# Performance work log

Measured on AMD Instinct MI355X. Metric: run time of the kernel, lower is better.

Reference implementation:

```python
import jax, jax.numpy as jnp
import numpy as np

S, B, D, NH, DH, L, V, DI = 1024, 4, 768, 12, 64, 4, 32000, 3072


def layer_norm(x, g, b, eps=1e-5):
    mu = jnp.mean(x, axis=-1, keepdims=True)
    var = jnp.mean((x - mu) ** 2, axis=-1, keepdims=True)
    return (x - mu) * jax.lax.rsqrt(var + eps) * g + b


def sinusoid_pos_emb():
    # PositionalEmbedding: ger(pos_seq, inv_freq) then [sin, cos]
    pos_seq = jnp.arange(S - 1, -1, -1, dtype=jnp.float32)
    inv_freq = 1.0 / (10000.0 ** (jnp.arange(0.0, D, 2.0) / D))
    si = pos_seq[:, None] * inv_freq[None, :]
    return jnp.concatenate([jnp.sin(si), jnp.cos(si)], axis=-1)  # (S, D)


def setup_inputs() -> dict:
    key = jax.random.key(0)
    ks = jax.random.split(key, 16)
    w = 0.02
    inp = jax.random.randint(ks[0], (S, B), 0, V)
    word_emb = jax.random.normal(ks[1], (V, D)) * w
    Wq = jax.random.normal(ks[2], (L, D, D)) * w
    Wkv = jax.random.normal(ks[3], (L, 2 * D, D)) * w
    Wo = jax.random.normal(ks[4], (L, D, D)) * w
    ln1_g = jnp.ones((L, D)); ln1_b = jnp.zeros((L, D))
    ffW1 = jax.random.normal(ks[5], (L, DI, D)) * w
    ffb1 = jnp.zeros((L, DI))
    ffW2 = jax.random.normal(ks[6], (L, D, DI)) * w
    ffb2 = jnp.zeros((L, D))
    ln2_g = jnp.ones((L, D)); ln2_b = jnp.zeros((L, D))
    # pre-populated InfiniAttn memory state; norm kept strictly positive
    memory = jax.random.normal(ks[7], (L, B, NH, DH, DH)) * jnp.sqrt(jnp.float32(S))
    mem_norm = jax.random.uniform(ks[8], (L, B, NH, DH)) * S + 0.5 * S
    return dict(inp=inp, word_emb=word_emb, Wq=Wq, Wkv=Wkv, Wo=Wo,
                ln1_g=ln1_g, ln1_b=ln1_b, ffW1=ffW1, ffb1=ffb1,
                ffW2=ffW2, ffb2=ffb2, ln2_g=ln2_g, ln2_b=ln2_b,
                memory=memory, mem_norm=mem_norm)


def reference(inp, word_emb, Wq, Wkv, Wo, ln1_g, ln1_b, ffW1, ffb1, ffW2, ffb2,
              ln2_g, ln2_b, memory, mem_norm):
    emb_scale = D ** 0.5
    h = word_emb[inp] * emb_scale + sinusoid_pos_emb()[:, None, :]  # (S,B,D)
    causal = jnp.triu(jnp.ones((S, S), dtype=bool), k=1)  # mask j > i
    scale = 1.0 / DH ** 0.5
    gate = jax.nn.sigmoid(jnp.float32(0.01))  # sigmoid(beta), beta_eps=0.01 (buffer)
    neg_inf = jnp.finfo(h.dtype).min
    new_mems, new_norms = [], []
    for l in range(L):
        q = (h @ Wq[l].T).reshape(S, B, NH, DH)
        kv = h @ Wkv[l].T
        k, v = jnp.split(kv, 2, axis=-1)
        k = k.reshape(S, B, NH, DH)
        v = v.reshape(S, B, NH, DH)
        score = jnp.einsum('ibnd,jbnd->ijbn', q, k) * scale
        score = jnp.where(causal[:, :, None, None], neg_inf, score)
        prob = jax.nn.softmax(score, axis=1)
        attn_vec = jnp.einsum('ijbn,jbnd->ibnd', prob, v).reshape(S, B, NH * DH)
        # NOTE: original calls _update_memory(head_q, head_v, head_k), i.e. K=v, V=k
        Qb = jnp.swapaxes(q, 0, 1)  # (B,S,n,d)
        Kb = jnp.swapaxes(v, 0, 1)
        Vb = jnp.swapaxes(k, 0, 1)
        cQ = jax.nn.elu(Qb) + 1.0
        cK = jax.nn.elu(Kb) + 1.0
        # memory retrieval (detached in the original)
        num = jnp.einsum('bsnk,bnkv->bsnv', cQ, memory[l])
        den = jnp.einsum('bsnk,bnk->bsn', cQ, mem_norm[l])[..., None]
        content_A = jax.lax.stop_gradient(num / den)  # (B,S,n,d)
        # memory update with delta trick (no_grad in the original)
        numK = jnp.einsum('bsnk,bnkv->bsnv', cK, memory[l])
        denK = jnp.einsum('bsnk,bnk->bsn', cK, mem_norm[l])[..., None]
        delta = numK / denK
        new_mems.append(jax.lax.stop_gradient(
            memory[l] + jnp.einsum('bsnk,bsnv->bnkv', cK, Vb - delta)))
        new_norms.append(jax.lax.stop_gradient(mem_norm[l] + cK.sum(axis=1)))
        # gated injection of memory content into local attention output
        attn_vec = gate * jnp.swapaxes(content_A, 0, 1).reshape(S, B, NH * DH) \
                   + (1.0 - gate) * attn_vec
        out = layer_norm(h + attn_vec @ Wo[l].T, ln1_g[l], ln1_b[l])
        core = jax.nn.relu(out @ ffW1[l].T + ffb1[l]) @ ffW2[l].T + ffb2[l]
        h = layer_norm(out + core, ln2_g[l], ln2_b[l])
    return h, jnp.stack(new_mems), jnp.stack(new_norms)
```

## Files before the change

kernel.cpp:

```cpp
#include <hip/hip_runtime.h>
#include <hip/hip_bf16.h>
#include <math.h>

#define S 1024
#define B 4
#define Dm 768
#define NH 12
#define DH 64
#define NL 4
#define DI 3072
#define QS 2304
#define MU_CHUNK 8

typedef __hip_bfloat16 bf16;
typedef short bf16x8 __attribute__((ext_vector_type(8)));
typedef float f32x4 __attribute__((ext_vector_type(4)));

__device__ __forceinline__ float b2f(bf16 x) { return __bfloat162float(x); }
__device__ __forceinline__ bf16 f2b(float x) { return __float2bfloat16(x); }

__device__ __forceinline__ float ldv(const float* p, size_t i) { return p[i]; }
__device__ __forceinline__ float ldv(const bf16* p, size_t i) { return b2f(p[i]); }

__device__ __forceinline__ float wave_sum(float x) {
  #pragma unroll
  for (int off = 32; off > 0; off >>= 1) x += __shfl_xor(x, off, 64);
  return x;
}

typedef const __attribute__((address_space(1))) unsigned int guint;
typedef __attribute__((address_space(3))) unsigned int luint;
__device__ __forceinline__ void async_cp16(const void* g, void* l) {
  __builtin_amdgcn_global_load_lds((guint*)g, (luint*)l, 16, 0, 0);
}

__global__ void embed_kernel(const int* __restrict__ inp, const float* __restrict__ wemb,
                             float* __restrict__ h, bf16* __restrict__ hb) {
  int idx = blockIdx.x * blockDim.x + threadIdx.x;
  if (idx >= S * B * Dm) return;
  int d = idx % Dm;
  int sb = idx / Dm;
  int b = sb % B;
  int s = sb / B;
  int tok = inp[s * B + b];
  float e = wemb[(size_t)tok * Dm + d] * 27.712812921102035f;
  float ps = (float)(S - 1 - s);
  float pe;
  if (d < Dm / 2) {
    float invf = expf(-(2.0f * (float)d / (float)Dm) * 9.210340371976184f);
    pe = sinf(ps * invf);
  } else {
    int j = d - Dm / 2;
    float invf = expf(-(2.0f * (float)j / (float)Dm) * 9.210340371976184f);
    pe = cosf(ps * invf);
  }
  float val = e + pe;
  h[idx] = val;
  hb[idx] = f2b(val);
}

#define SEG_QKV 1769472
#define SEG_WO  2359296
#define SEG_W1  4718592
#define SEG_END 7077888
__global__ void convw_kernel(const float* __restrict__ Wq, const float* __restrict__ Wkv,
                             const float* __restrict__ Wo, const float* __restrict__ W1,
                             const float* __restrict__ W2, bf16* __restrict__ dst) {
  int idx = (blockIdx.x * blockDim.x + threadIdx.x) * 4;
  if (idx >= SEG_END) return;
  const float* src;
  if (idx < SEG_QKV) {
    src = (idx < 589824) ? Wq + idx : Wkv + (idx - 589824);
  } else if (idx < SEG_WO) {
    src = Wo + (idx - SEG_QKV);
  } else if (idx < SEG_W1) {
    src = W1 + (idx - SEG_WO);
  } else {
    src = W2 + (idx - SEG_W1);
  }
  float4 f = *(const float4*)src;
  bf16 b0 = f2b(f.x), b1 = f2b(f.y), b2 = f2b(f.z), b3 = f2b(f.w);
  unsigned short o[4];
  o[0] = *(unsigned short*)&b0; o[1] = *(unsigned short*)&b1;
  o[2] = *(unsigned short*)&b2; o[3] = *(unsigned short*)&b3;
  *(uint2*)((unsigned short*)dst + idx) = *(uint2*)o;
}

template <int MREP, int RELU>
__global__ __launch_bounds__(256) void gemm_async(const bf16* __restrict__ A,
                                                  const bf16* __restrict__ W,
                                                  const float* __restrict__ bias,
                                                  bf16* __restrict__ C,
                                                  int ldc, int K) {
  constexpr int BM = MREP * 32;
  __shared__ __align__(16) unsigned short Asm[BM * 32];
  __shared__ __align__(16) unsigned short Bsm[128 * 32];
  const int t = threadIdx.x;
  const int w = t >> 6, lane = t & 63;
  const int col = lane & 15, quad = lane >> 4;
  const int wm = w >> 1, wn = w & 1;
  const int m0 = blockIdx.y * BM, n0 = blockIdx.x * 128;

  const bf16* aSrc = A + (size_t)(m0 + w * 16 + col) * K + quad * 8;
  const bf16* bSrc = W + (size_t)(n0 + w * 16 + col) * K + quad * 8;

  const f32x4 zf = {0.0f, 0.0f, 0.0f, 0.0f};
  f32x4 acc[MREP][4];
  #pragma unroll
  for (int mt = 0; mt < MREP; mt++)
    #pragma unroll
    for (int nt = 0; nt < 4; nt++) acc[mt][nt] = zf;

  for (int kk = 0; kk < K; kk += 32) {
    __syncthreads();
    #pragma unroll
    for (int i = 0; i < MREP / 2; i++)
      async_cp16(aSrc + kk + (size_t)i * 64 * K, &Asm[i * 2048 + w * 512]);
    #pragma unroll
    for (int i = 0; i < 2; i++)
      async_cp16(bSrc + kk + (size_t)i * 64 * K, &Bsm[i * 2048 + w * 512]);
    __syncthreads();
    bf16x8 af[MREP], bfr[4];
    #pragma unroll
    for (int mt = 0; mt < MREP; mt++)
      af[mt] = *(const bf16x8*)&Asm[(wm * MREP + mt) * 512 + lane * 8];
    #pragma unroll
    for (int nt = 0; nt < 4; nt++)
      bfr[nt] = *(const bf16x8*)&Bsm[(wn * 4 + nt) * 512 + lane * 8];
    #pragma unroll
    for (int mt = 0; mt < MREP; mt++)
      #pragma unroll
      for (int nt = 0; nt < 4; nt++)
        acc[mt][nt] = __builtin_amdgcn_mfma_f32_16x16x32_bf16(af[mt], bfr[nt],
                                                              acc[mt][nt], 0, 0, 0);
  }

  #pragma unroll
  for (int nt = 0; nt < 4; nt++) {
    const int colg = n0 + wn * 64 + nt * 16 + col;
    const float bv = bias ? bias[colg] : 0.0f;
    #pragma unroll
    for (int mt = 0; mt < MREP; mt++) {
      #pragma unroll
      for (int r = 0; r < 4; r++) {
        const int row = m0 + wm * (MREP * 16) + mt * 16 + quad * 4 + r;
        float val = acc[mt][nt][r] + bv;
        if (RELU) val = fmaxf(val, 0.0f);
        C[(size_t)row * ldc + colg] = f2b(val);
      }
    }
  }
}

__global__ __launch_bounds__(256) void attn_flash(const bf16* __restrict__ q,
                                                  const bf16* __restrict__ k,
                                                  const bf16* __restrict__ v,
                                                  bf16* __restrict__ att) {
  const int it = blockIdx.x;
  const int bn = blockIdx.y;
  const int b = bn / NH, n = bn % NH;
  const int t = threadIdx.x;
  const int w = t >> 6, lane = t & 63;
  const int col = lane & 15, quad = lane >> 4;
  const int i0 = it * 64;

  __shared__ __align__(16) unsigned short Kt[64 * 72];
  __shared__ __align__(16) unsigned short Vt[64 * 72];
  __shared__ __align__(16) unsigned short Pw[64 * 72];

  const unsigned short* qp = (const unsigned short*)q;
  const unsigned short* kp = (const unsigned short*)k;
  const unsigned short* vp = (const unsigned short*)v;

  bf16x8 aq[2];
  {
    size_t qb = ((size_t)(i0 + w * 16 + col) * B + b) * QS + n * DH + quad * 8;
    aq[0] = *(const bf16x8*)(qp + qb);
    aq[1] = *(const bf16x8*)(qp + qb + 32);
  }

  const f32x4 zf = {0.0f, 0.0f, 0.0f, 0.0f};
  float mrow[4], lrow[4];
  f32x4 o[4];
  #pragma unroll
  for (int r = 0; r < 4; r++) { mrow[r] = -1e30f; lrow[r] = 0.0f; }
  #pragma unroll
  for (int db = 0; db < 4; db++) o[db] = zf;

  const int jj = t >> 2;
  const int d0 = (t & 3) << 4;

  for (int jt = 0; jt <= it; jt++) {
    const int j0 = jt * 64;
    __syncthreads();
    {
      size_t gb = ((size_t)(j0 + jj) * B + b) * QS + n * DH + d0;
      *(uint4*)&Kt[jj * 72 + d0] = *(const uint4*)(kp + gb);
      *(uint4*)&Kt[jj * 72 + d0 + 8] = *(const uint4*)(kp + gb + 8);
      unsigned short tv[16];
      *(uint4*)tv = *(const uint4*)(vp + gb);
      *(uint4*)(tv + 8) = *(const uint4*)(vp + gb + 8);
      #pragma unroll
      for (int x = 0; x < 16; x++) Vt[(d0 + x) * 72 + jj] = tv[x];
    }
    __syncthreads();

    f32x4 sf[4];
    #pragma unroll
    for (int nb = 0; nb < 4; nb++) sf[nb] = zf;
    #pragma unroll
    for (int ks = 0; ks < 2; ks++) {
      #pragma unroll
      for (int nb = 0; nb < 4; nb++) {
        bf16x8 kb = *(const bf16x8*)&Kt[(nb * 16 + col) * 72 + ks * 32 + quad * 8];
        sf[nb] = __builtin_amdgcn_mfma_f32_16x16x32_bf16(aq[ks], kb, sf[nb], 0, 0, 0);
      }
    }

    const bool diag = (jt == it);
    #pragma unroll
    for (int r = 0; r < 4; r++) {
      const int irow = i0 + w * 16 + quad * 4 + r;
      float sv[4];
      #pragma unroll
      for (int nb = 0; nb < 4; nb++) {
        float s = sf[nb][r] * 0.125f;
        if (diag && (j0 + nb * 16 + col) > irow) s = -1e30f;
        sv[nb] = s;
      }
      float rm = fmaxf(fmaxf(sv[0], sv[1]), fmaxf(sv[2], sv[3]));
      #pragma unroll
      for (int off = 8; off > 0; off >>= 1) rm = fmaxf(rm, __shfl_xor(rm, off, 64));
      const float mn = fmaxf(mrow[r], rm);
      const float alpha = __expf(mrow[r] - mn);
      mrow[r] = mn;
      float ps = 0.0f;
      #pragma unroll
      for (int nb = 0; nb < 4; nb++) {
        float p = __expf(sv[nb] - mn);
        ps += p;
        bf16 hb = f2b(p);
        Pw[(w * 16 + quad * 4 + r) * 72 + nb * 16 + col] = *(unsigned short*)&hb;
      }
      #pragma unroll
      for (int off = 8; off > 0; off >>= 1) ps += __shfl_xor(ps, off, 64);
      lrow[r] = lrow[r] * alpha + ps;
      #pragma unroll
      for (int db = 0; db < 4; db++) o[db][r] *= alpha;
    }

    #pragma unroll
    for (int ks = 0; ks < 2; ks++) {
      bf16x8 pa = *(const bf16x8*)&Pw[(w * 16 + col) * 72 + ks * 32 + quad * 8];
      #pragma unroll
      for (int db = 0; db < 4; db++) {
        bf16x8 vb = *(const bf16x8*)&Vt[(db * 16 + col) * 72 + ks * 32 + quad * 8];
        o[db] = __builtin_amdgcn_mfma_f32_16x16x32_bf16(pa, vb, o[db], 0, 0, 0);
      }
    }
  }

  unsigned short* ap = (unsigned short*)att;
  #pragma unroll
  for (int r = 0; r < 4; r++) {
    const int irow = i0 + w * 16 + quad * 4 + r;
    const float inv = 1.0f / lrow[r];
    size_t ob = ((size_t)irow * B + b) * Dm + n * DH + col;
    #pragma unroll
    for (int db = 0; db < 4; db++) {
      bf16 hb = f2b(o[db][r] * inv);
      ap[ob + db * 16] = *(unsigned short*)&hb;
    }
  }
}

__global__ __launch_bounds__(256) void meminfer_mfma(const bf16* __restrict__ qkv,
                                                     const float* __restrict__ mem,
                                                     const float* __restrict__ mnorm,
                                                     bf16* __restrict__ att,
                                                     bf16* __restrict__ vd) {
  const int s0 = blockIdx.x * 64;
  const int bn = blockIdx.y;
  const int b = bn / NH, n = bn % NH;
  const int t = threadIdx.x;
  const int w = t >> 6, lane = t & 63;
  const int col = lane & 15, quad = lane >> 4;

  __shared__ __align__(16) unsigned short CQ[4096];
  __shared__ __align__(16) unsigned short CK[4096];
  __shared__ __align__(16) unsigned short Bm[5120];

  const unsigned short* qp = (const unsigned short*)qkv;

  {
    int r = t >> 2;
    int k0 = (t & 3) * 16;
    size_t gb = ((size_t)(s0 + r) * B + b) * QS + n * DH + k0;
    int abase = (r >> 4) * 1024 + (k0 >> 5) * 512 + ((k0 & 31) >> 3) * 128 + (r & 15) * 8;
    unsigned short tq[16], tv[16], oq[16], ov[16];
    *(uint4*)tq = *(const uint4*)(qp + gb);
    *(uint4*)(tq + 8) = *(const uint4*)(qp + gb + 8);
    *(uint4*)tv = *(const uint4*)(qp + gb + 1536);
    *(uint4*)(tv + 8) = *(const uint4*)(qp + gb + 1536 + 8);
    #pragma unroll
    for (int i = 0; i < 16; i++) {
      float fq = b2f(*(const bf16*)&tq[i]);
      float fv = b2f(*(const bf16*)&tv[i]);
      float eq = fq > 0.0f ? fq + 1.0f : __expf(fq);
      float ev = fv > 0.0f ? fv + 1.0f : __expf(fv);
      bf16 bq = f2b(eq), bv2 = f2b(ev);
      oq[i] = *(unsigned short*)&bq;
      ov[i] = *(unsigned short*)&bv2;
    }
    *(bf16x8*)&CQ[abase] = *(bf16x8*)oq;
    *(bf16x8*)&CQ[abase + 128] = *(bf16x8*)(oq + 8);
    *(bf16x8*)&CK[abase] = *(bf16x8*)ov;
    *(bf16x8*)&CK[abase + 128] = *(bf16x8*)(ov + 8);
  }
  {
    int v = t & 63, kb = (t >> 6) * 16;
    const float* mp = mem + (size_t)bn * DH * DH;
    #pragma unroll
    for (int i = 0; i < 16; i++) {
      int k = kb + i;
      bf16 mb = f2b(mp[(size_t)k * DH + v]);
      int addr = (v >> 4) * 1024 + (k >> 5) * 512 + ((k & 31) >> 3) * 128 + (v & 15) * 8 + (k & 7);
      Bm[addr] = *(unsigned short*)&mb;
    }
  }
  {
    int a = t * 4;
    int m = (a >> 3) & 15;
    int kk = (a >> 9) * 32 + ((a >> 7) & 3) * 8 + (a & 7);
    unsigned short vals[4] = {0, 0, 0, 0};
    if (m == 0) {
      const float* np = mnorm + (size_t)bn * DH;
      #pragma unroll
      for (int j = 0; j < 4; j++) {
        bf16 nb = f2b(np[kk + j]);
        vals[j] = *(unsigned short*)&nb;
      }
    }
    *(uint2*)&Bm[4096 + a] = *(uint2*)vals;
  }
  __syncthreads();

  const f32x4 zf = {0.0f, 0.0f, 0.0f, 0.0f};
  f32x4 aq[5], ak[5];
  #pragma unroll
  for (int nb = 0; nb < 5; nb++) { aq[nb] = zf; ak[nb] = zf; }
  #pragma unroll
  for (int ks = 0; ks < 2; ks++) {
    bf16x8 fq = *(const bf16x8*)&CQ[w * 1024 + ks * 512 + lane * 8];
    bf16x8 fk = *(const bf16x8*)&CK[w * 1024 + ks * 512 + lane * 8];
    #pragma unroll
    for (int nb = 0; nb < 5; nb++) {
      bf16x8 bm = *(const bf16x8*)&Bm[nb * 1024 + ks * 512 + lane * 8];
      aq[nb] = __builtin_amdgcn_mfma_f32_16x16x32_bf16(fq, bm, aq[nb], 0, 0, 0);
      ak[nb] = __builtin_amdgcn_mfma_f32_16x16x32_bf16(fk, bm, ak[nb], 0, 0, 0);
    }
  }

  const float gate = 1.0f / (1.0f + expf(-0.01f));
  unsigned short* ap = (unsigned short*)att;
  unsigned short* vp2 = (unsigned short*)vd;
  #pragma unroll
  for (int r = 0; r < 4; r++) {
    const int srow = s0 + w * 16 + quad * 4 + r;
    const float denq = __shfl(aq[4][r], lane & 48, 64);
    const float denk = __shfl(ak[4][r], lane & 48, 64);
    const size_t bd = ((size_t)srow * B + b) * Dm + n * DH + col;
    const size_t bq = ((size_t)srow * B + b) * QS + 768 + n * DH + col;
    #pragma unroll
    for (int nb = 0; nb < 4; nb++) {
      float content = aq[nb][r] / denq;
      float delta = ak[nb][r] / denk;
      float attv = b2f(*(const bf16*)&ap[bd + nb * 16]);
      bf16 ao = f2b(gate * content + (1.0f - gate) * attv);
      ap[bd + nb * 16] = *(unsigned short*)&ao;
      float kvv = b2f(*(const bf16*)&qp[bq + nb * 16]);
      bf16 vo = f2b(kvv - delta);
      vp2[bd + nb * 16] = *(unsigned short*)&vo;
    }
  }
}

__global__ void memupd_kernel(const bf16* __restrict__ qkv, const bf16* __restrict__ vd,
                              float* __restrict__ part, float* __restrict__ pnorm) {
  int bn = blockIdx.x % (B * NH);
  int c = blockIdx.x / (B * NH);
  int b = bn / NH, n = bn % NH;
  int t = threadIdx.x;
  int k = t >> 2;
  int v0 = (t & 3) * 16;
  __shared__ float ckl[8][DH];
  __shared__ float vdl[8][DH];
  float acc[16];
  #pragma unroll
  for (int j = 0; j < 16; j++) acc[j] = 0.0f;
  float nsum = 0.0f;
  const int sBeg = c * (S / MU_CHUNK), sEnd = sBeg + S / MU_CHUNK;
  for (int s0 = sBeg; s0 < sEnd; s0 += 8) {
    #pragma unroll
    for (int i2 = 0; i2 < 2; i2++) {
      int idx = t + i2 * 256;
      int sp = idx >> 6, dd = idx & 63;
      int gq = ((s0 + sp) * B + b) * QS + 1536 + n * DH + dd;
      int gd = ((s0 + sp) * B + b) * Dm + n * DH + dd;
      float vv = b2f(qkv[gq]);
      ckl[sp][dd] = vv > 0.0f ? vv + 1.0f : expf(vv);
      vdl[sp][dd] = b2f(vd[gd]);
    }
    __syncthreads();
    #pragma unroll
    for (int sp = 0; sp < 8; sp++) {
      float cc = ckl[sp][k];
      if ((t & 3) == 0) nsum += cc;
      #pragma unroll
      for (int j = 0; j < 16; j++) acc[j] += cc * vdl[sp][v0 + j];
    }
    __syncthreads();
  }
  float* prow = part + (size_t)c * (B * NH * DH * DH) + (size_t)bn * DH * DH;
  #pragma unroll
  for (int j4 = 0; j4 < 4; j4++) {
    float4 o;
    o.x = acc[j4 * 4 + 0]; o.y = acc[j4 * 4 + 1];
    o.z = acc[j4 * 4 + 2]; o.w = acc[j4 * 4 + 3];
    *(float4*)&prow[k * DH + v0 + j4 * 4] = o;
  }
  if ((t & 3) == 0) pnorm[(size_t)c * (B * NH * DH) + bn * DH + k] = nsum;
}

__global__ void memred_kernel(const float* __restrict__ mem, const float* __restrict__ mnorm,
                              const float* __restrict__ part, const float* __restrict__ pnorm,
                              float* __restrict__ out_mem, float* __restrict__ out_norm) {
  const int MEMN = B * NH * DH * DH;
  int i = blockIdx.x * blockDim.x + threadIdx.x;
  if (i < MEMN / 4) {
    int i4 = i * 4;
    float4 a = *(const float4*)(mem + i4);
    #pragma unroll
    for (int c = 0; c < MU_CHUNK; c++) {
      float4 p = *(const float4*)(part + (size_t)c * MEMN + i4);
      a.x += p.x; a.y += p.y; a.z += p.z; a.w += p.w;
    }
    *(float4*)(out_mem + i4) = a;
  } else {
    int j4 = (i - MEMN / 4) * 4;
    if (j4 < B * NH * DH) {
      float4 a = *(const float4*)(mnorm + j4);
      #pragma unroll
      for (int c = 0; c < MU_CHUNK; c++) {
        float4 p = *(const float4*)(pnorm + (size_t)c * (B * NH * DH) + j4);
        a.x += p.x; a.y += p.y; a.z += p.z; a.w += p.w;
      }
      *(float4*)(out_norm + j4) = a;
    }
  }
}

template <typename TX, typename TY>
__global__ void addln_kernel(const TX* __restrict__ x, const TY* __restrict__ y,
                             const float* __restrict__ g, const float* __restrict__ bb,
                             float* __restrict__ outf, bf16* __restrict__ outb) {
  int row = blockIdx.x;
  int t = threadIdx.x;
  float vals[3];
  float sum = 0.0f, sq = 0.0f;
  #pragma unroll
  for (int i = 0; i < 3; i++) {
    size_t idx = (size_t)row * Dm + t + i * 256;
    float vv = ldv(x, idx) + ldv(y, idx);
    vals[i] = vv;
    sum += vv;
    sq += vv * vv;
  }
  sum = wave_sum(sum);
  sq = wave_sum(sq);
  __shared__ float s1[4], s2[4];
  int w = t >> 6, lane = t & 63;
  if (lane == 0) { s1[w] = sum; s2[w] = sq; }
  __syncthreads();
  if (t == 0) {
    s1[0] = s1[0] + s1[1] + s1[2] + s1[3];
    s2[0] = s2[0] + s2[1] + s2[2] + s2[3];
  }
  __syncthreads();
  sum = s1[0]; sq = s2[0];
  float mu = sum / 768.0f;
  float var = sq / 768.0f - mu * mu;
  float rs = rsqrtf(var + 1e-5f);
  #pragma unroll
  for (int i = 0; i < 3; i++) {
    int d = t + i * 256;
    float o = (vals[i] - mu) * rs * g[d] + bb[d];
    size_t idx = (size_t)row * Dm + d;
    if (outf) outf[idx] = o;
    if (outb) outb[idx] = f2b(o);
  }
}

extern "C" void kernel_launch(void* const* d_in, const int* in_sizes, int n_in,
                              void* d_out, int out_size, void* d_ws, size_t ws_size,
                              hipStream_t stream) {
  (void)in_sizes; (void)n_in; (void)out_size; (void)ws_size;
  const int*   inp   = (const int*)d_in[0];
  const float* wemb  = (const float*)d_in[1];
  const float* Wq    = (const float*)d_in[2];
  const float* Wkv   = (const float*)d_in[3];
  const float* Wo    = (const float*)d_in[4];
  const float* ln1g  = (const float*)d_in[5];
  const float* ln1b  = (const float*)d_in[6];
  const float* fW1   = (const float*)d_in[7];
  const float* fb1   = (const float*)d_in[8];
  const float* fW2   = (const float*)d_in[9];
  const float* fb2   = (const float*)d_in[10];
  const float* ln2g  = (const float*)d_in[11];
  const float* ln2b  = (const float*)d_in[12];
  const float* mem   = (const float*)d_in[13];
  const float* mnorm = (const float*)d_in[14];

  const size_t SBD = (size_t)S * B * Dm;

  bf16* ws   = (bf16*)d_ws;
  bf16* qkv  = ws;
  bf16* vd   = ws + 3 * SBD;
  bf16* att  = ws + 4 * SBD;
  bf16* hbf  = att;
  bf16* ff2o = att;
  bf16* out1 = ws + 5 * SBD;
  bf16* wb   = ws + 6 * SBD;
  bf16* ffm  = ws;
  bf16* tmp  = ws;
  float* part  = (float*)out1;
  float* pnorm = (float*)(wb + SEG_END);

  float* h    = (float*)d_out;
  float* outm = h + SBD;
  float* outn = outm + (size_t)NL * B * NH * DH * DH;

  dim3 b256(256);
  embed_kernel<<<dim3((S * B * Dm + 255) / 256), b256, 0, stream>>>(inp, wemb, h, hbf);

  for (int l = 0; l < NL; l++) {
    convw_kernel<<<dim3(SEG_END / 4 / 256), b256, 0, stream>>>(
        Wq + (size_t)l * Dm * Dm, Wkv + (size_t)l * 2 * Dm * Dm,
        Wo + (size_t)l * Dm * Dm, fW1 + (size_t)l * DI * Dm,
        fW2 + (size_t)l * Dm * DI, wb);
    const bf16* wqkv = wb;
    const bf16* wo_b = wb + SEG_QKV;
    const bf16* w1_b = wb + SEG_WO;
    const bf16* w2_b = wb + SEG_W1;
    const float* mem_l = mem + (size_t)l * B * NH * DH * DH;
    const float* mn_l  = mnorm + (size_t)l * B * NH * DH;
    float* outm_l = outm + (size_t)l * B * NH * DH * DH;
    float* outn_l = outn + (size_t)l * B * NH * DH;

    gemm_async<4, 0><<<dim3(QS / 128, 32), b256, 0, stream>>>(hbf, wqkv, nullptr, qkv, QS, Dm);

    attn_flash<<<dim3(S / 64, B * NH), b256, 0, stream>>>(qkv, qkv + 768, qkv + 1536, att);
    meminfer_mfma<<<dim3(S / 64, B * NH), b256, 0, stream>>>(qkv, mem_l, mn_l, att, vd);
    memupd_kernel<<<dim3(B * NH * MU_CHUNK), b256, 0, stream>>>(qkv, vd, part, pnorm);
    memred_kernel<<<dim3(771), b256, 0, stream>>>(mem_l, mn_l, part, pnorm, outm_l, outn_l);

    gemm_async<2, 0><<<dim3(Dm / 128, 64), b256, 0, stream>>>(att, wo_b, nullptr, tmp, Dm, Dm);
    addln_kernel<float, bf16><<<dim3(S * B), b256, 0, stream>>>(
        h, tmp, ln1g + l * Dm, ln1b + l * Dm, nullptr, out1);

    gemm_async<4, 1><<<dim3(DI / 128, 32), b256, 0, stream>>>(out1, w1_b, fb1 + (size_t)l * DI,
                                                              ffm, DI, Dm);
    gemm_async<2, 0><<<dim3(Dm / 128, 64), b256, 0, stream>>>(ffm, w2_b, fb2 + (size_t)l * Dm,
                                                              ff2o, Dm, DI);
    addln_kernel<bf16, bf16><<<dim3(S * B), b256, 0, stream>>>(
        out1, ff2o, ln2g + l * Dm, ln2b + l * Dm, h, hbf);
  }
}
```

Measured before the change: 1.375 ms.

## Double-buffer GEMM shared tiles and add split-K for narrow-output GEMMs

The GEMM kernel now double-buffers its A and B shared-memory tiles, so the async copy for the next K step is issued before the MFMAs on the current tile, with one barrier per iteration instead of two. The Wo and FFN2 GEMMs, which have only 6x64 output tiles, are split over K into two slices that write fp32 partial sums. A separate reduce kernel adds the slices, applies the bias and converts to bf16. This aims to hide load latency and put more blocks on the device, at the cost of extra fp32 partial-sum traffic, an extra launch per split GEMM, and double the LDS per block.

```diff
diff --git a/kernel.cpp b/kernel.cpp
--- a/kernel.cpp
+++ b/kernel.cpp
@@ -86,23 +86,25 @@
   *(uint2*)((unsigned short*)dst + idx) = *(uint2*)o;
 }
 
-template <int MREP, int RELU>
+template <int MREP, int RELU, int SPLITK, typename OT>
 __global__ __launch_bounds__(256) void gemm_async(const bf16* __restrict__ A,
                                                   const bf16* __restrict__ W,
                                                   const float* __restrict__ bias,
-                                                  bf16* __restrict__ C,
+                                                  OT* __restrict__ C,
                                                   int ldc, int K) {
   constexpr int BM = MREP * 32;
-  __shared__ __align__(16) unsigned short Asm[BM * 32];
-  __shared__ __align__(16) unsigned short Bsm[128 * 32];
+  __shared__ __align__(16) unsigned short Asm[2][BM * 32];
+  __shared__ __align__(16) unsigned short Bsm[2][128 * 32];
   const int t = threadIdx.x;
   const int w = t >> 6, lane = t & 63;
   const int col = lane & 15, quad = lane >> 4;
   const int wm = w >> 1, wn = w & 1;
   const int m0 = blockIdx.y * BM, n0 = blockIdx.x * 128;
-
-  const bf16* aSrc = A + (size_t)(m0 + w * 16 + col) * K + quad * 8;
-  const bf16* bSrc = W + (size_t)(n0 + w * 16 + col) * K + quad * 8;
+  const int Kc = K / SPLITK;
+  const int kbeg = (SPLITK > 1) ? blockIdx.z * Kc : 0;
+
+  const bf16* aSrc = A + (size_t)(m0 + w * 16 + col) * K + kbeg + quad * 8;
+  const bf16* bSrc = W + (size_t)(n0 + w * 16 + col) * K + kbeg + quad * 8;
 
   const f32x4 zf = {0.0f, 0.0f, 0.0f, 0.0f};
   f32x4 acc[MREP][4];
@@ -111,30 +113,57 @@
     #pragma unroll
     for (int nt = 0; nt < 4; nt++) acc[mt][nt] = zf;
 
-  for (int kk = 0; kk < K; kk += 32) {
-    __syncthreads();
+  #pragma unroll
+  for (int i = 0; i < MREP / 2; i++)
+    async_cp16(aSrc + (size_t)i * 64 * K, &Asm[0][i * 2048 + w * 512]);
+  #pragma unroll
+  for (int i = 0; i < 2; i++)
+    async_cp16(bSrc + (size_t)i * 64 * K, &Bsm[0][i * 2048 + w * 512]);
+  __syncthreads();
+
+  int cur = 0;
+  for (int kk = 32; kk < Kc; kk += 32) {
     #pragma unroll
     for (int i = 0; i < MREP / 2; i++)
-      async_cp16(aSrc + kk + (size_t)i * 64 * K, &Asm[i * 2048 + w * 512]);
+      async_cp16(aSrc + kk + (size_t)i * 64 * K, &Asm[cur ^ 1][i * 2048 + w * 512]);
     #pragma unroll
     for (int i = 0; i < 2; i++)
-      async_cp16(bSrc + kk + (size_t)i * 64 * K, &Bsm[i * 2048 + w * 512]);
-    __syncthreads();
+      async_cp16(bSrc + kk + (size_t)i * 64 * K, &Bsm[cur ^ 1][i * 2048 + w * 512]);
     bf16x8 af[MREP], bfr[4];
     #pragma unroll
     for (int mt = 0; mt < MREP; mt++)
-      af[mt] = *(const bf16x8*)&Asm[(wm * MREP + mt) * 512 + lane * 8];
+      af[mt] = *(const bf16x8*)&Asm[cur][(wm * MREP + mt) * 512 + lane * 8];
     #pragma unroll
     for (int nt = 0; nt < 4; nt++)
-      bfr[nt] = *(const bf16x8*)&Bsm[(wn * 4 + nt) * 512 + lane * 8];
+      bfr[nt] = *(const bf16x8*)&Bsm[cur][(wn * 4 + nt) * 512 + lane * 8];
     #pragma unroll
     for (int mt = 0; mt < MREP; mt++)
       #pragma unroll
       for (int nt = 0; nt < 4; nt++)
         acc[mt][nt] = __builtin_amdgcn_mfma_f32_16x16x32_bf16(af[mt], bfr[nt],
                                                               acc[mt][nt], 0, 0, 0);
-  }
-
+    __syncthreads();
+    cur ^= 1;
+  }
+  {
+    bf16x8 af[MREP], bfr[4];
+    #pragma unroll
+    for (int mt = 0; mt < MREP; mt++)
+      af[mt] = *(const bf16x8*)&Asm[cur][(wm * MREP + mt) * 512 + lane * 8];
+    #pragma unroll
+    for (int nt = 0; nt < 4; nt++)
+      bfr[nt] = *(const bf16x8*)&Bsm[cur][(wn * 4 + nt) * 512 + lane * 8];
+    #pragma unroll
+    for (int mt = 0; mt < MREP; mt++)
+      #pragma unroll
+      for (int nt = 0; nt < 4; nt++)
+        acc[mt][nt] = __builtin_amdgcn_mfma_f32_16x16x32_bf16(af[mt], bfr[nt],
+                                                              acc[mt][nt], 0, 0, 0);
+  }
+
+  OT* Cb = C;
+  if (SPLITK > 1)
+    Cb = C + (size_t)blockIdx.z * gridDim.y * BM * ldc;
   #pragma unroll
   for (int nt = 0; nt < 4; nt++) {
     const int colg = n0 + wn * 64 + nt * 16 + col;
@@ -146,10 +175,40 @@
         const int row = m0 + wm * (MREP * 16) + mt * 16 + quad * 4 + r;
         float val = acc[mt][nt][r] + bv;
         if (RELU) val = fmaxf(val, 0.0f);
-        C[(size_t)row * ldc + colg] = f2b(val);
+        if constexpr (__is_same(OT, float)) {
+          Cb[(size_t)row * ldc + colg] = val;
+        } else {
+          Cb[(size_t)row * ldc + colg] = f2b(val);
+        }
       }
     }
   }
+}
+
+template <int NSLICE, int RELU>
+__global__ void gemmred_kernel(const float* __restrict__ part, const float* __restrict__ bias,
+                               bf16* __restrict__ out, int N, size_t MN) {
+  size_t i4 = ((size_t)blockIdx.x * blockDim.x + threadIdx.x) * 4;
+  if (i4 >= MN) return;
+  float4 a = *(const float4*)(part + i4);
+  #pragma unroll
+  for (int z = 1; z < NSLICE; z++) {
+    float4 p = *(const float4*)(part + (size_t)z * MN + i4);
+    a.x += p.x; a.y += p.y; a.z += p.z; a.w += p.w;
+  }
+  if (bias) {
+    int colb = (int)(i4 % N);
+    a.x += bias[colb]; a.y += bias[colb + 1]; a.z += bias[colb + 2]; a.w += bias[colb + 3];
+  }
+  if (RELU) {
+    a.x = fmaxf(a.x, 0.0f); a.y = fmaxf(a.y, 0.0f);
+    a.z = fmaxf(a.z, 0.0f); a.w = fmaxf(a.w, 0.0f);
+  }
+  bf16 b0 = f2b(a.x), b1 = f2b(a.y), b2 = f2b(a.z), b3 = f2b(a.w);
+  unsigned short o[4];
+  o[0] = *(unsigned short*)&b0; o[1] = *(unsigned short*)&b1;
+  o[2] = *(unsigned short*)&b2; o[3] = *(unsigned short*)&b3;
+  *(uint2*)((unsigned short*)out + i4) = *(uint2*)o;
 }
 
 __global__ __launch_bounds__(256) void attn_flash(const bf16* __restrict__ q,
@@ -504,7 +563,7 @@
 extern "C" void kernel_launch(void* const* d_in, const int* in_sizes, int n_in,
                               void* d_out, int out_size, void* d_ws, size_t ws_size,
                               hipStream_t stream) {
-  (void)in_sizes; (void)n_in; (void)out_size; (void)ws_size;
+  (void)in_sizes; (void)n_in; (void)out_size;
   const int*   inp   = (const int*)d_in[0];
   const float* wemb  = (const float*)d_in[1];
   const float* Wq    = (const float*)d_in[2];
@@ -535,6 +594,10 @@
   bf16* tmp  = ws;
   float* part  = (float*)out1;
   float* pnorm = (float*)(wb + SEG_END);
+  float* partg = pnorm + (size_t)MU_CHUNK * B * NH * DH;
+  const size_t need = ((size_t)(6 * SBD + SEG_END)) * 2 +
+                      ((size_t)MU_CHUNK * B * NH * DH + 2 * SBD) * 4;
+  const bool use_splitk = (ws_size >= need);
 
   float* h    = (float*)d_out;
   float* outm = h + SBD;
@@ -557,21 +620,37 @@
     float* outm_l = outm + (size_t)l * B * NH * DH * DH;
     float* outn_l = outn + (size_t)l * B * NH * DH;
 
-    gemm_async<4, 0><<<dim3(QS / 128, 32), b256, 0, stream>>>(hbf, wqkv, nullptr, qkv, QS, Dm);
+    gemm_async<4, 0, 1, bf16><<<dim3(QS / 128, 32), b256, 0, stream>>>(
+        hbf, wqkv, nullptr, qkv, QS, Dm);
 
     attn_flash<<<dim3(S / 64, B * NH), b256, 0, stream>>>(qkv, qkv + 768, qkv + 1536, att);
     meminfer_mfma<<<dim3(S / 64, B * NH), b256, 0, stream>>>(qkv, mem_l, mn_l, att, vd);
     memupd_kernel<<<dim3(B * NH * MU_CHUNK), b256, 0, stream>>>(qkv, vd, part, pnorm);
     memred_kernel<<<dim3(771), b256, 0, stream>>>(mem_l, mn_l, part, pnorm, outm_l, outn_l);
 
-    gemm_async<2, 0><<<dim3(Dm / 128, 64), b256, 0, stream>>>(att, wo_b, nullptr, tmp, Dm, Dm);
+    if (use_splitk) {
+      gemm_async<2, 0, 2, float><<<dim3(Dm / 128, 64, 2), b256, 0, stream>>>(
+          att, wo_b, nullptr, partg, Dm, Dm);
+      gemmred_kernel<2, 0><<<dim3((unsigned)(SBD / 4 / 256)), b256, 0, stream>>>(
+          partg, nullptr, tmp, Dm, SBD);
+    } else {
+      gemm_async<2, 0, 1, bf16><<<dim3(Dm / 128, 64), b256, 0, stream>>>(
+          att, wo_b, nullptr, tmp, Dm, Dm);
+    }
     addln_kernel<float, bf16><<<dim3(S * B), b256, 0, stream>>>(
         h, tmp, ln1g + l * Dm, ln1b + l * Dm, nullptr, out1);
 
-    gemm_async<4, 1><<<dim3(DI / 128, 32), b256, 0, stream>>>(out1, w1_b, fb1 + (size_t)l * DI,
-                                                              ffm, DI, Dm);
-    gemm_async<2, 0><<<dim3(Dm / 128, 64), b256, 0, stream>>>(ffm, w2_b, fb2 + (size_t)l * Dm,
-                                                              ff2o, Dm, DI);
+    gemm_async<4, 1, 1, bf16><<<dim3(DI / 128, 32), b256, 0, stream>>>(
+        out1, w1_b, fb1 + (size_t)l * DI, ffm, DI, Dm);
+    if (use_splitk) {
+      gemm_async<2, 0, 2, float><<<dim3(Dm / 128, 64, 2), b256, 0, stream>>>(
+          ffm, w2_b, nullptr, partg, Dm, DI);
+      gemmred_kernel<2, 0><<<dim3((unsigned)(SBD / 4 / 256)), b256, 0, stream>>>(
+          partg, fb2 + (size_t)l * Dm, ff2o, Dm, SBD);
+    } else {
+      gemm_async<2, 0, 1, bf16><<<dim3(Dm / 128, 64), b256, 0, stream>>>(
+          ffm, w2_b, fb2 + (size_t)l * Dm, ff2o, Dm, DI);
+    }
     addln_kernel<bf16, bf16><<<dim3(S * B), b256, 0, stream>>>(
         out1, ff2o, ln2g + l * Dm, ln2b + l * Dm, h, hbf);
   }
```

After: 1.326 ms. 3.6% less time.
